# Kernel optimization log

Measured on AMD Instinct MI355X. Metric: run time of the kernel, lower is better.

## Reference

```python
import jax, jax.numpy as jnp
import numpy as np

NUM_EXPERTS = 16
TOP_K = 2
FFT_LEN = 512
SEQ_LEN = 512
PRED_LEN = 720
MOE_TEMP = 1.0


def setup_inputs() -> dict:
    key = jax.random.key(0)
    ks = jax.random.split(key, 5)
    x = jax.random.normal(ks[0], (8192, SEQ_LEN), dtype=jnp.float32)
    # gating network: Linear(fft_len//2 -> num_experts)
    gw = jax.random.normal(ks[1], (NUM_EXPERTS, FFT_LEN // 2), dtype=jnp.float32) * (1.0 / np.sqrt(FFT_LEN // 2))
    gb = jnp.zeros((NUM_EXPERTS,), dtype=jnp.float32)
    # experts: RLinear = instance-norm (RevIN) + Linear(seq->pred), stacked
    ew = jax.random.normal(ks[2], (NUM_EXPERTS, SEQ_LEN, PRED_LEN), dtype=jnp.float32) * (1.0 / np.sqrt(SEQ_LEN))
    eb = jnp.zeros((NUM_EXPERTS, PRED_LEN), dtype=jnp.float32)
    return {"x": x, "gw": gw, "gb": gb, "ew": ew, "eb": eb}


def periodogram(x, n):
    # x: [B, L] -> normalized power spectrum [B, n//2]
    x0 = x - jnp.mean(x, axis=1, keepdims=True)
    dft = jnp.fft.fft(x0, n=n, axis=1) / jnp.sqrt(jnp.asarray(n, x.dtype))
    I = jnp.abs(dft[:, : n // 2]) ** 2
    s = jnp.sum(I, axis=1, keepdims=True)
    s = jnp.where(s == 0, 1.0, s)
    return I / s


def expert_apply(x, ew, eb):
    # RLinear: instance normalize, linear map, de-normalize
    mu = jnp.mean(x, axis=1, keepdims=True)
    sd = jnp.std(x, axis=1, keepdims=True) + 1e-5
    xn = (x - mu) / sd  # [B, L]
    # all experts densely: [B,L] x [E,L,P] -> [E,B,P]
    y = jnp.einsum('bl,elp->ebp', xn, ew) + eb[:, None, :]
    return y * sd[None] + mu[None]  # [E, B, P]


def reference(x, gw, gb, ew, eb):
    I = periodogram(x, FFT_LEN)  # [B, n//2]
    gate = (I @ gw.T + gb) / MOE_TEMP  # eval mode: divide by temp, no noise
    topk_vals, topk_idx = jax.lax.top_k(gate, TOP_K)  # [B, k]
    gates = jax.nn.softmax(topk_vals, axis=1)  # [B, k]
    expert_out = expert_apply(x, ew, eb)  # [E, B, P]
    # gather selected experts: [B, k, P]
    sel = jnp.take_along_axis(
        jnp.transpose(expert_out, (1, 0, 2)), topk_idx[:, :, None], axis=1
    )
    return jnp.sum(gates[:, :, None] * sel, axis=1)  # [B, P]
```

## Files before the change

### kernel.cpp

```cpp
#include <hip/hip_runtime.h>
#include <hip/hip_bf16.h>
#include <math.h>

#define NEXP  16
#define SEQ   512
#define PRED  720
#define NROWS 8192
#define NFREQ 256

typedef __bf16 bf16x8 __attribute__((ext_vector_type(8)));
typedef float  f32x16 __attribute__((ext_vector_type(16)));

__device__ __forceinline__ void gload_lds16(const void* g, void* l) {
    __builtin_amdgcn_global_load_lds(
        (const __attribute__((address_space(1))) unsigned int*)g,
        (__attribute__((address_space(3))) unsigned int*)l, 16, 0, 0);
}

__device__ __forceinline__ int xcd_swizzle(int bid, int nwg) {
    const int q = nwg >> 3, r = nwg & 7;
    const int xcd = bid & 7, off = bid >> 3;
    return (xcd < r ? xcd * (q + 1) : r * (q + 1) + (xcd - r) * q) + off;
}

__global__ __launch_bounds__(256) void k_preproc(const float* __restrict__ ew,
                                                 const float* __restrict__ x,
                                                 __hip_bfloat16* __restrict__ ewt,
                                                 __hip_bfloat16* __restrict__ bthi,
                                                 __hip_bfloat16* __restrict__ btlo,
                                                 __hip_bfloat16* __restrict__ xn,
                                                 __hip_bfloat16* __restrict__ xnlo,
                                                 float* __restrict__ meta,
                                                 int* __restrict__ nredo)
{
    const int bid = blockIdx.x;
    const int t   = threadIdx.x;

    if (bid < 512) {
        if (bid == 0 && t == 0) *nredo = 0;
        const int tid  = bid * 256 + t;
        const int f    = tid >> 9;
        const int lidx = tid & 511;
        const int m    = (f * lidx) & 511;

        constexpr double Cj[9] = {0.9999247018391445033, 0.9996988186962042201,
                                  0.9987954562051723927, 0.9951847266721968862,
                                  0.9807852804032304491, 0.9238795325112867561,
                                  0.7071067811865475244, 0.0, -1.0};
        constexpr double Sj[9] = {0.0122715382857199261, 0.0245412285229122880,
                                  0.0490676743274180143, 0.0980171403295606020,
                                  0.1950903220161282678, 0.3826834323650897717,
                                  0.7071067811865475244, 1.0, 0.0};
        double cr = 1.0, ci = 0.0;
#pragma unroll
        for (int j = 0; j < 9; ++j) {
            const bool on = (m >> j) & 1;
            const double mr = on ? Cj[j] : 1.0;
            const double mi = on ? Sj[j] : 0.0;
            const double nr = cr * mr - ci * mi;
            ci = cr * mi + ci * mr;
            cr = nr;
        }
        const size_t c0 = (size_t)(2 * f) * 512 + lidx;
        const size_t c1 = (size_t)(2 * f + 1) * 512 + lidx;
        {
            __hip_bfloat16 h = __float2bfloat16((float)cr);
            float hif = __bfloat162float(h);
            bthi[c0] = h;
            btlo[c0] = __float2bfloat16((float)(cr - (double)hif));
        }
        {
            __hip_bfloat16 h = __float2bfloat16((float)ci);
            float hif = __bfloat162float(h);
            bthi[c1] = h;
            btlo[c1] = __float2bfloat16((float)(ci - (double)hif));
        }
        return;
    }

    if (bid < 6400) {
        __shared__ float tile[32][33];
        const int rel = bid - 512;
        const int e   = rel / 368;
        const int rem = rel % 368;
        const int p0  = (rem % 23) * 32;
        const int l0  = (rem / 23) * 32;
        const int tx  = t & 31;
        const int ty  = t >> 5;
        const float* src = ew + (size_t)e * SEQ * PRED;
#pragma unroll
        for (int i = 0; i < 4; ++i) {
            int l = l0 + ty + i * 8;
            int p = p0 + tx;
            tile[ty + i * 8][tx] = (p < PRED) ? src[(size_t)l * PRED + p] : 0.f;
        }
        __syncthreads();
        __hip_bfloat16* dst = ewt + (size_t)e * PRED * SEQ;
#pragma unroll
        for (int i = 0; i < 4; ++i) {
            int p = p0 + ty + i * 8;
            int l = l0 + tx;
            if (p < PRED) dst[(size_t)p * SEQ + l] = __float2bfloat16(tile[tx][ty + i * 8]);
        }
        return;
    }

    {
        const int wv = t >> 6, l = t & 63;
        const int b  = (bid - 6400) * 4 + wv;
        const float* xr = x + (size_t)b * SEQ;

        const float4 v0 = *(const float4*)(xr + l * 8);
        const float4 v1 = *(const float4*)(xr + l * 8 + 4);
        const double d0 = v0.x, d1 = v0.y, d2 = v0.z, d3 = v0.w;
        const double d4 = v1.x, d5 = v1.y, d6 = v1.z, d7 = v1.w;

        double s1 = ((d0 + d1) + (d2 + d3)) + ((d4 + d5) + (d6 + d7));
        double s2 = ((d0 * d0 + d1 * d1) + (d2 * d2 + d3 * d3)) +
                    ((d4 * d4 + d5 * d5) + (d6 * d6 + d7 * d7));
#pragma unroll
        for (int off = 1; off < 64; off <<= 1) {
            s1 += __shfl_xor(s1, off);
            s2 += __shfl_xor(s2, off);
        }
        const double mu = s1 * (1.0 / 512.0);
        double var = s2 * (1.0 / 512.0) - mu * mu;
        if (var < 0.0) var = 0.0;
        const double sd = sqrt(var) + 1e-5, inv = 1.0 / sd;

        unsigned int hw[4], lw[4];
#define CONV(j, dj)                                                         \
        {                                                                   \
            double xnd = (dj - mu) * inv;                                   \
            __hip_bfloat16 h = __float2bfloat16((float)xnd);                \
            float hif = __bfloat162float(h);                                \
            __hip_bfloat16 lo = __float2bfloat16((float)(xnd - (double)hif)); \
            unsigned int hb = *(unsigned short*)&h;                         \
            unsigned int lb = *(unsigned short*)&lo;                        \
            if ((j & 1) == 0) { hw[j >> 1] = hb; lw[j >> 1] = lb; }         \
            else { hw[j >> 1] |= hb << 16; lw[j >> 1] |= lb << 16; }        \
        }
        CONV(0, d0) CONV(1, d1) CONV(2, d2) CONV(3, d3)
        CONV(4, d4) CONV(5, d5) CONV(6, d6) CONV(7, d7)
#undef CONV
        *(uint4*)(xn   + (size_t)b * SEQ + l * 8) = uint4{hw[0], hw[1], hw[2], hw[3]};
        *(uint4*)(xnlo + (size_t)b * SEQ + l * 8) = uint4{lw[0], lw[1], lw[2], lw[3]};

        if (l == 0) {
            meta[b * 4 + 0] = (float)mu;
            meta[b * 4 + 3] = (float)sd;
        }
    }
}

__global__ __launch_bounds__(256, 3) void k_dft_gemm(
    const __hip_bfloat16* __restrict__ xn, const __hip_bfloat16* __restrict__ xnlo,
    const __hip_bfloat16* __restrict__ bthi, const __hip_bfloat16* __restrict__ btlo,
    float* __restrict__ Iout)
{
    const int wgid = xcd_swizzle(blockIdx.x, 512);
    const int rt = wgid >> 2;
    const int ct = wgid & 3;

    __shared__ __align__(16) __hip_bfloat16 As[2][64][64];
    __shared__ __align__(16) __hip_bfloat16 Bs[2][128][64];

    const int t  = threadIdx.x;
    const int wv = t >> 6, l = t & 63;

    size_t aoff[2], boff[4];
    int arow[2], achk[2], brow[4], bchk[4];
#pragma unroll
    for (int i = 0; i < 2; ++i) {
        const int idx = i * 256 + t;
        const int row = idx >> 3, chk = idx & 7;
        const int swz = (row & 7) ^ ((row & 8) >> 1);
        arow[i] = row; achk[i] = chk;
        aoff[i] = (size_t)(rt * 64 + row) * SEQ + (size_t)(chk ^ swz) * 8;
    }
#pragma unroll
    for (int i = 0; i < 4; ++i) {
        const int idx = i * 256 + t;
        const int row = idx >> 3, chk = idx & 7;
        const int swz = (row & 7) ^ ((row & 8) >> 1);
        brow[i] = row; bchk[i] = chk;
        boff[i] = (size_t)(ct * 128 + row) * SEQ + (size_t)(chk ^ swz) * 8;
    }

#define DSTAGE(buf, kk) do {                                                   \
    const int pass_ = (kk) >> 3;                                               \
    const int koff_ = ((kk) & 7) * 64;                                         \
    const __hip_bfloat16* ap_ = (pass_ == 1) ? xnlo : xn;                      \
    const __hip_bfloat16* bp_ = (pass_ == 2) ? btlo : bthi;                    \
    _Pragma("unroll")                                                          \
    for (int i_ = 0; i_ < 2; ++i_)                                             \
        gload_lds16(ap_ + aoff[i_] + koff_, &As[buf][arow[i_]][achk[i_] * 8]); \
    _Pragma("unroll")                                                          \
    for (int i_ = 0; i_ < 4; ++i_)                                             \
        gload_lds16(bp_ + boff[i_] + koff_, &Bs[buf][brow[i_]][bchk[i_] * 8]); \
} while (0)

    f32x16 acc[2];
#pragma unroll
    for (int ni = 0; ni < 2; ++ni)
#pragma unroll
        for (int q = 0; q < 16; ++q) acc[ni][q] = 0.f;

    const int wr = wv >> 1, wc = wv & 1;
    const int fl = l & 31, fh = l >> 5;
    const int rswz = (fl & 7) ^ ((fl & 8) >> 1);

    DSTAGE(0, 0);
    asm volatile("s_waitcnt vmcnt(0)" ::: "memory");
    __builtin_amdgcn_s_barrier();
#pragma unroll
    for (int kt = 0; kt < 24; ++kt) {
        const int cur = kt & 1;
        if (kt < 23) DSTAGE(cur ^ 1, kt + 1);
        __builtin_amdgcn_sched_barrier(0);
        __builtin_amdgcn_s_setprio(1);
#pragma unroll
        for (int ks = 0; ks < 4; ++ks) {
            const int cc = ((ks * 2 + fh) ^ rswz) * 8;
            const bf16x8 a  = *(const bf16x8*)&As[cur][wr * 32 + fl][cc];
            const bf16x8 b0 = *(const bf16x8*)&Bs[cur][wc * 64 + fl][cc];
            const bf16x8 b1 = *(const bf16x8*)&Bs[cur][wc * 64 + 32 + fl][cc];
            acc[0] = __builtin_amdgcn_mfma_f32_32x32x16_bf16(a, b0, acc[0], 0, 0, 0);
            acc[1] = __builtin_amdgcn_mfma_f32_32x32x16_bf16(a, b1, acc[1], 0, 0, 0);
        }
        __builtin_amdgcn_s_setprio(0);
        __builtin_amdgcn_sched_barrier(0);
        asm volatile("s_waitcnt vmcnt(0)" ::: "memory");
        __builtin_amdgcn_s_barrier();
    }
#undef DSTAGE

    const int crow_base = 4 * fh;
#pragma unroll
    for (int ni = 0; ni < 2; ++ni) {
        const int col = ct * 128 + wc * 64 + ni * 32 + fl;
#pragma unroll
        for (int q = 0; q < 16; ++q) {
            const float v = acc[ni][q];
            const float w = __shfl_xor(v, 1);
            if ((fl & 1) == 0) {
                const int rl = wr * 32 + (q & 3) + 8 * (q >> 2) + crow_base;
                Iout[(size_t)(rt * 64 + rl) * NFREQ + (col >> 1)] = v * v + w * w;
            }
        }
    }
}

__global__ __launch_bounds__(256) void k_gatefin(const float* __restrict__ Iout,
                                                 const float* __restrict__ gw,
                                                 const float* __restrict__ gb,
                                                 float* __restrict__ meta,
                                                 int* __restrict__ eidx,
                                                 int* __restrict__ redo,
                                                 int* __restrict__ nredo)
{
    __shared__ float gws[NEXP * 257];
    __shared__ float Pw[4][256];
    __shared__ float Gs[4][16];

    const int t  = threadIdx.x;
    const int wv = t >> 6, l = t & 63;
    const int b  = blockIdx.x * 4 + wv;

    for (int i = t; i < NEXP * NFREQ; i += 256)
        gws[(i >> 8) * 257 + (i & 255)] = gw[i];
    __syncthreads();

    const float* Ir = Iout + (size_t)b * NFREQ;
    const float i0 = Ir[l], i1 = Ir[64 + l], i2 = Ir[128 + l], i3 = Ir[192 + l];
    Pw[wv][l] = i0; Pw[wv][64 + l] = i1; Pw[wv][128 + l] = i2; Pw[wv][192 + l] = i3;
    float ps = (i0 + i1) + (i2 + i3);
#pragma unroll
    for (int off = 1; off < 64; off <<= 1) ps += __shfl_xor(ps, off);

    const int e = l >> 2, kb = l & 3;
    float acc = 0.f;
#pragma unroll 8
    for (int j = 0; j < 64; ++j) {
        const int k = kb + 4 * j;
        acc += Pw[wv][k] * gws[e * 257 + k];
    }
    acc += __shfl_xor(acc, 1);
    acc += __shfl_xor(acc, 2);
    if (kb == 0) Gs[wv][e] = acc;

    if (l == 0) {
        const float sdiv  = (ps == 0.f) ? 1.f : ps;
        const float inv_s = 1.f / sdiv;
        float b1 = -1e30f, b2 = -1e30f, b3 = -1e30f;
        int i1b = 0, i2b = 0;
#pragma unroll
        for (int i = 0; i < NEXP; ++i) {
            float v = Gs[wv][i] * inv_s + gb[i];
            if (v > b1)      { b3 = b2; b2 = b1; i2b = i1b; b1 = v; i1b = i; }
            else if (v > b2) { b3 = b2; b2 = v; i2b = i; }
            else if (v > b3) { b3 = v; }
        }
        if (b2 - b3 < 1e-4f * fmaxf(1.f, fabsf(b1))) {
            const int r = atomicAdd(nredo, 1);
            redo[r] = b;
        } else {
            const float sd = meta[b * 4 + 3];
            const float ee = __expf(b2 - b1);
            const float w0 = 1.f / (1.f + ee);
            const float w1 = ee / (1.f + ee);
            meta[b * 4 + 1] = w0 * sd;
            meta[b * 4 + 2] = w1 * sd;
            eidx[b * 2 + 0] = i1b;
            eidx[b * 2 + 1] = i2b;
        }
    }
}

__global__ __launch_bounds__(256, 4) void k_gate64(const float* __restrict__ x,
                                                   const float* __restrict__ gw,
                                                   const float* __restrict__ gb,
                                                   float* __restrict__ meta,
                                                   int* __restrict__ eidx,
                                                   const int* __restrict__ redo,
                                                   const int* __restrict__ nredo)
{
    __shared__ double Pw[4][256];
    __shared__ double Gs[4][16];

    const int t  = threadIdx.x;
    const int wv = t >> 6, l = t & 63;
    const int n  = *nredo;

    for (int it = blockIdx.x * 4 + wv; it < n; it += gridDim.x * 4) {
        const int b = redo[it];
        const float* xr = x + (size_t)b * SEQ;

        double s1 = 0.0, s2 = 0.0;
#define DLOADV(n_) double vr##n_ = (double)xr[64 * n_ + l]; s1 += vr##n_; s2 += vr##n_ * vr##n_;
        DLOADV(0) DLOADV(1) DLOADV(2) DLOADV(3) DLOADV(4) DLOADV(5) DLOADV(6) DLOADV(7)
#undef DLOADV
        double vi0, vi1, vi2, vi3, vi4, vi5, vi6, vi7;

#pragma unroll
        for (int off = 1; off < 64; off <<= 1) {
            s1 += __shfl_xor(s1, off);
            s2 += __shfl_xor(s2, off);
        }
        const double mu = s1 * (1.0 / 512.0);
        double var = s2 * (1.0 / 512.0) - mu * mu;
        if (var < 0.0) var = 0.0;
        const double sd = sqrt(var) + 1e-5;

#define DSUB(n_) vr##n_ -= mu;
        DSUB(0) DSUB(1) DSUB(2) DSUB(3) DSUB(4) DSUB(5) DSUB(6) DSUB(7)
#undef DSUB

        {
            const double C = 0.70710678118654752440084436210485;
            double a0 = vr0 + vr4, a1 = vr1 + vr5, a2 = vr2 + vr6, a3 = vr3 + vr7;
            double d0 = vr0 - vr4, d1 = vr1 - vr5, d2 = vr2 - vr6, d3 = vr3 - vr7;
            double c0 = a0 + a2, c2 = a0 - a2, c1 = a1 + a3;
            double c3i = a3 - a1;
            double e1r = C * (d1 - d3), e1i = -C * (d1 + d3);
            vr0 = c0 + c1;   vi0 = 0.0;
            vr1 = c0 - c1;   vi1 = 0.0;
            vr2 = c2;        vi2 = c3i;
            vr3 = c2;        vi3 = -c3i;
            vr4 = d0 + e1r;  vi4 = -d2 + e1i;
            vr5 = d0 - e1r;  vi5 = -d2 - e1i;
            vr6 = d0 - e1r;  vi6 =  d2 + e1i;
            vr7 = d0 + e1r;  vi7 =  d2 - e1i;
        }

        double w1r = 1.0, w1i = 0.0;
        {
            constexpr double Cr[6] = {0.9999247018391445033, 0.9996988186962042201,
                                      0.9987954562051723927, 0.9951847266721968862,
                                      0.9807852804032304491, 0.9238795325112867561};
            constexpr double Ci[6] = {-0.0122715382857199261, -0.0245412285229122880,
                                      -0.0490676743274180143, -0.0980171403295606020,
                                      -0.1950903220161282678, -0.3826834323650897717};
#pragma unroll
            for (int j = 0; j < 6; ++j) {
                const bool on = (l >> j) & 1;
                const double mr = on ? Cr[j] : 1.0;
                const double mi = on ? Ci[j] : 0.0;
                const double nr = w1r * mr - w1i * mi;
                w1i = w1r * mi + w1i * mr;
                w1r = nr;
            }
        }

        {
            double wkr = w1r, wki = w1i;
#define DTWID(n_) { double tr_ = vr##n_ * wkr - vi##n_ * wki; \
                    vi##n_ = vr##n_ * wki + vi##n_ * wkr; vr##n_ = tr_; }
#define DWSTEP() { double nr_ = wkr * w1r - wki * w1i; \
                   wki = wkr * w1i + wki * w1r; wkr = nr_; }
            DTWID(4) DWSTEP() DTWID(2) DWSTEP() DTWID(6) DWSTEP() DTWID(1)
            DWSTEP() DTWID(5) DWSTEP() DTWID(3) DWSTEP() DTWID(7)
#undef DTWID
#undef DWSTEP
        }

        double twr, twi;
        {
            double w2r = w1r * w1r - w1i * w1i, w2i = 2.0 * w1r * w1i;
            double w4r = w2r * w2r - w2i * w2i, w4i = 2.0 * w2r * w2i;
            twr = w4r * w4r - w4i * w4i; twi = 2.0 * w4r * w4i;
        }
#define DBF(R, I, h, hi, ter, tei) { \
        double br_ = __shfl_xor(R, h); double bi_ = __shfl_xor(I, h); \
        double dr_ = hi ? (R - br_) : (R + br_); \
        double di_ = hi ? (I - bi_) : (I + bi_); \
        R = dr_ * ter - di_ * tei; I = dr_ * tei + di_ * ter; }
#define DSTG(hc) { \
        const bool hi_ = (l & hc) != 0; \
        const double ter_ = hi_ ? twr : 1.0; \
        const double tei_ = hi_ ? twi : 0.0; \
        DBF(vr0, vi0, hc, hi_, ter_, tei_) DBF(vr1, vi1, hc, hi_, ter_, tei_) \
        DBF(vr2, vi2, hc, hi_, ter_, tei_) DBF(vr3, vi3, hc, hi_, ter_, tei_) \
        DBF(vr4, vi4, hc, hi_, ter_, tei_) DBF(vr5, vi5, hc, hi_, ter_, tei_) \
        DBF(vr6, vi6, hc, hi_, ter_, tei_) DBF(vr7, vi7, hc, hi_, ter_, tei_) \
        double ntr_ = twr * twr - twi * twi; twi = 2.0 * twr * twi; twr = ntr_; }
        DSTG(32) DSTG(16) DSTG(8) DSTG(4) DSTG(2) DSTG(1)
#undef DSTG
#undef DBF

        const int k2 = (int)(__brev((unsigned)l) >> 26);
        double ps = 0.0;
        if ((l & 1) == 0) {
            const int kb = 8 * k2;
            double P;
            P = vr0 * vr0 + vi0 * vi0; ps += P; Pw[wv][0 + kb] = P;
            P = vr1 * vr1 + vi1 * vi1; ps += P; Pw[wv][4 + kb] = P;
            P = vr2 * vr2 + vi2 * vi2; ps += P; Pw[wv][2 + kb] = P;
            P = vr3 * vr3 + vi3 * vi3; ps += P; Pw[wv][6 + kb] = P;
            P = vr4 * vr4 + vi4 * vi4; ps += P; Pw[wv][1 + kb] = P;
            P = vr5 * vr5 + vi5 * vi5; ps += P; Pw[wv][5 + kb] = P;
            P = vr6 * vr6 + vi6 * vi6; ps += P; Pw[wv][3 + kb] = P;
            P = vr7 * vr7 + vi7 * vi7; ps += P; Pw[wv][7 + kb] = P;
        }
#pragma unroll
        for (int off = 1; off < 64; off <<= 1) ps += __shfl_xor(ps, off);

        {
            const int e = l >> 2, kb = l & 3;
            double acc = 0.0;
#pragma unroll 8
            for (int j = 0; j < 64; ++j) {
                int k = kb + 4 * j;
                acc += Pw[wv][k] * (double)gw[e * NFREQ + k];
            }
            acc += __shfl_xor(acc, 1);
            acc += __shfl_xor(acc, 2);
            if (kb == 0) Gs[wv][e] = acc;
        }

        if (l == 0) {
            const double sdiv  = (ps == 0.0) ? 1.0 : ps;
            const double inv_s = 1.0 / sdiv;
            double best = -1e300, best2 = -1e300;
            int i0b = 0, i1b = 0;
#pragma unroll
            for (int i = 0; i < NEXP; ++i) {
                double v = Gs[wv][i] * inv_s + (double)gb[i];
                if (v > best)       { best2 = best; i1b = i0b; best = v; i0b = i; }
                else if (v > best2) { best2 = v; i1b = i; }
            }
            const double eexp = (double)__expf((float)(best2 - best));
            const double w0 = 1.0 / (1.0 + eexp);
            const double w1 = eexp / (1.0 + eexp);
            meta[b * 4 + 0] = (float)mu;
            meta[b * 4 + 1] = (float)(w0 * sd);
            meta[b * 4 + 2] = (float)(w1 * sd);
            meta[b * 4 + 3] = (float)sd;
            eidx[b * 2 + 0] = i0b;
            eidx[b * 2 + 1] = i1b;
        }
    }
}

__global__ __launch_bounds__(256) void k_count(const int* __restrict__ eidx,
                                               int* __restrict__ blockHist)
{
    __shared__ int h[32];
    const int t   = threadIdx.x;
    const int blk = blockIdx.x;
    if (t < 32) h[t] = 0;
    __syncthreads();
    const int b  = blk * 256 + t;
    const int e0 = eidx[2 * b];
    const int e1 = eidx[2 * b + 1];
    atomicAdd(&h[e0], 1);
    atomicAdd(&h[16 + e1], 1);
    __syncthreads();
    if (t < 32) blockHist[(t >> 4) * 512 + blk * 16 + (t & 15)] = h[t];
}

__global__ void k_scan(const int* __restrict__ blockHist, int* __restrict__ counts,
                       int* __restrict__ offs, int* __restrict__ tdesc,
                       int* __restrict__ base)
{
    __shared__ int cnt[32];
    __shared__ int off_s[32];
    const int j = threadIdx.x;
    if (j < 32) {
        const int s = j >> 4, e = j & 15;
        int acc = 0;
        for (int blk = 0; blk < 32; ++blk) acc += blockHist[s * 512 + blk * 16 + e];
        cnt[j] = acc;
        counts[j] = acc;
    }
    __syncthreads();
    if (j < 2) {
        int acc = 0, tt = 0;
        for (int i = 0; i < NEXP; ++i) {
            const int c = cnt[j * 16 + i];
            off_s[j * 16 + i] = acc;
            offs[j * 16 + i]  = acc;
            acc += c;
            const int nt = (c + 63) >> 6;
            for (int k = 0; k < nt; ++k) tdesc[j * 160 + tt++] = (i << 16) | k;
        }
        for (; tt < 160; ++tt) tdesc[j * 160 + tt] = -1;
    }
    __syncthreads();
    if (j < 32) {
        const int s = j >> 4, e = j & 15;
        int run = off_s[j];
        for (int blk = 0; blk < 32; ++blk) {
            base[s * 512 + blk * 16 + e] = run;
            run += blockHist[s * 512 + blk * 16 + e];
        }
    }
}

__global__ __launch_bounds__(256) void k_scatter(const int* __restrict__ eidx,
                                                 const int* __restrict__ base,
                                                 int* __restrict__ lists)
{
    __shared__ int whist[2][4][16];
    const int t   = threadIdx.x;
    const int wv  = t >> 6, l = t & 63;
    const int blk = blockIdx.x;
    const int b   = blk * 256 + t;
    const int e0  = eidx[2 * b];
    const int e1  = eidx[2 * b + 1];
    const unsigned long long before = (1ULL << l) - 1ULL;

    unsigned long long m0 = 0, m1 = 0;
#pragma unroll
    for (int bb = 0; bb < 16; ++bb) {
        unsigned long long m = __ballot(e0 == bb);
        if (e0 == bb) m0 = m;
        if (l == 0) whist[0][wv][bb] = __popcll(m);
    }
#pragma unroll
    for (int bb = 0; bb < 16; ++bb) {
        unsigned long long m = __ballot(e1 == bb);
        if (e1 == bb) m1 = m;
        if (l == 0) whist[1][wv][bb] = __popcll(m);
    }
    __syncthreads();

    int p0 = __popcll(m0 & before);
    int p1 = __popcll(m1 & before);
    for (int w = 0; w < 4; ++w) {
        if (w < wv) {
            p0 += whist[0][w][e0];
            p1 += whist[1][w][e1];
        }
    }
    lists[base[blk * 16 + e0] + p0]                 = b;
    lists[NROWS + base[512 + blk * 16 + e1] + p1]   = b;
}

__global__ __launch_bounds__(256, 3) void k_expert_gemm(
    const __hip_bfloat16* __restrict__ xn, const __hip_bfloat16* __restrict__ ewt,
    const float* __restrict__ eb, const float* __restrict__ meta,
    const int* __restrict__ lists, const int* __restrict__ offs,
    const int* __restrict__ counts, const int* __restrict__ tdesc,
    float* __restrict__ out, float* __restrict__ out2)
{
    const int wgid = xcd_swizzle(blockIdx.x, 1920);
    const int slot = wgid / 960;
    const int rem  = wgid - slot * 960;
    const int tid  = rem / 6;
    const int ct   = rem % 6;
    const int d    = tdesc[slot * 160 + tid];
    if (d < 0) return;
    const int e  = d >> 16;
    const int rt = d & 0xffff;
    const int n_e = counts[slot * NEXP + e];

    __shared__ __align__(16) __hip_bfloat16 As[2][64][64];
    __shared__ __align__(16) __hip_bfloat16 Bs[2][128][64];
    __shared__ int   rowB[64];
    __shared__ float rowMu[64];
    __shared__ float rowC[64];

    const int t  = threadIdx.x;
    const int wv = t >> 6, l = t & 63;
    const int* list = lists + slot * NROWS + offs[slot * NEXP + e];
    if (t < 64) {
        int r  = rt * 64 + t;
        int bb = (r < n_e) ? list[r] : -1;
        rowB[t]  = bb;
        rowMu[t] = (bb >= 0) ? meta[bb * 4] : 0.f;
        rowC[t]  = (bb >= 0) ? meta[bb * 4 + 1 + slot] : 0.f;
    }
    __syncthreads();

    const __hip_bfloat16* asrc[2];
    const __hip_bfloat16* bsrc[4];
    int arow[2], achk[2], brow[4], bchk[4];
#pragma unroll
    for (int i = 0; i < 2; ++i) {
        const int idx = i * 256 + t;
        const int row = idx >> 3, chk = idx & 7;
        const int swz = (row & 7) ^ ((row & 8) >> 1);
        arow[i] = row; achk[i] = chk;
        const int ab = rowB[row];
        asrc[i] = xn + ((ab >= 0) ? (size_t)ab * SEQ : 0) + (size_t)(chk ^ swz) * 8;
    }
#pragma unroll
    for (int i = 0; i < 4; ++i) {
        const int idx = i * 256 + t;
        const int row = idx >> 3, chk = idx & 7;
        const int swz = (row & 7) ^ ((row & 8) >> 1);
        brow[i] = row; bchk[i] = chk;
        const int gc  = ct * 128 + row;
        const int gcc = (gc < PRED) ? gc : (PRED - 1);
        bsrc[i] = ewt + ((size_t)e * PRED + gcc) * SEQ + (size_t)(chk ^ swz) * 8;
    }

#define STAGE(buf, koff) do {                                                  \
    _Pragma("unroll")                                                          \
    for (int i_ = 0; i_ < 2; ++i_)                                             \
        gload_lds16(asrc[i_] + (koff), &As[buf][arow[i_]][achk[i_] * 8]);      \
    _Pragma("unroll")                                                          \
    for (int i_ = 0; i_ < 4; ++i_)                                             \
        gload_lds16(bsrc[i_] + (koff), &Bs[buf][brow[i_]][bchk[i_] * 8]);      \
} while (0)

    f32x16 acc[2];
#pragma unroll
    for (int ni = 0; ni < 2; ++ni)
#pragma unroll
        for (int q = 0; q < 16; ++q) acc[ni][q] = 0.f;

    const int wr = wv >> 1, wc = wv & 1;
    const int fl = l & 31, fh = l >> 5;
    const int rswz = (fl & 7) ^ ((fl & 8) >> 1);

    STAGE(0, 0);
    asm volatile("s_waitcnt vmcnt(0)" ::: "memory");
    __builtin_amdgcn_s_barrier();
#pragma unroll
    for (int kt = 0; kt < 8; ++kt) {
        const int cur = kt & 1;
        if (kt < 7) STAGE(cur ^ 1, (kt + 1) * 64);
        __builtin_amdgcn_sched_barrier(0);
        __builtin_amdgcn_s_setprio(1);
#pragma unroll
        for (int ks = 0; ks < 4; ++ks) {
            const int cc = ((ks * 2 + fh) ^ rswz) * 8;
            const bf16x8 a  = *(const bf16x8*)&As[cur][wr * 32 + fl][cc];
            const bf16x8 b0 = *(const bf16x8*)&Bs[cur][wc * 64 + fl][cc];
            const bf16x8 b1 = *(const bf16x8*)&Bs[cur][wc * 64 + 32 + fl][cc];
            acc[0] = __builtin_amdgcn_mfma_f32_32x32x16_bf16(a, b0, acc[0], 0, 0, 0);
            acc[1] = __builtin_amdgcn_mfma_f32_32x32x16_bf16(a, b1, acc[1], 0, 0, 0);
        }
        __builtin_amdgcn_s_setprio(0);
        __builtin_amdgcn_sched_barrier(0);
        asm volatile("s_waitcnt vmcnt(0)" ::: "memory");
        __builtin_amdgcn_s_barrier();
    }
#undef STAGE

    const int crow_base = 4 * fh;
#pragma unroll
    for (int ni = 0; ni < 2; ++ni) {
        const int col = ct * 128 + wc * 64 + ni * 32 + fl;
        const bool cok = (col < PRED);
        const float ebv = cok ? eb[e * PRED + col] : 0.f;
#pragma unroll
        for (int q = 0; q < 16; ++q) {
            const int rl = wr * 32 + (q & 3) + 8 * (q >> 2) + crow_base;
            const int bb = rowB[rl];
            if (!cok || bb < 0) continue;
            const float v = acc[ni][q] + ebv;
            if (slot == 0) out [(size_t)bb * PRED + col] = rowMu[rl] + rowC[rl] * v;
            else           out2[(size_t)bb * PRED + col] = rowC[rl] * v;
        }
    }
}

__global__ __launch_bounds__(256) void k_merge(float* __restrict__ out,
                                               const float* __restrict__ out2)
{
    const int i = blockIdx.x * 256 + threadIdx.x;
    float4 a = ((float4*)out)[i];
    const float4 b = ((const float4*)out2)[i];
    a.x += b.x; a.y += b.y; a.z += b.z; a.w += b.w;
    ((float4*)out)[i] = a;
}

extern "C" void kernel_launch(void* const* d_in, const int* in_sizes, int n_in,
                              void* d_out, int out_size, void* d_ws, size_t ws_size,
                              hipStream_t stream)
{
    const float* x  = (const float*)d_in[0];
    const float* gw = (const float*)d_in[1];
    const float* gb = (const float*)d_in[2];
    const float* ew = (const float*)d_in[3];
    const float* eb = (const float*)d_in[4];
    float* out = (float*)d_out;
    char*  ws  = (char*)d_ws;

    constexpr size_t XN_OFF   = 0;
    constexpr size_t XN_SZ    = (size_t)NROWS * SEQ * 2;
    constexpr size_t XNLO_OFF = XN_OFF + XN_SZ;
    constexpr size_t EWT_OFF  = XNLO_OFF + XN_SZ;
    constexpr size_t EWT_SZ   = (size_t)NEXP * PRED * SEQ * 2;
    constexpr size_t BTHI_OFF = EWT_OFF + EWT_SZ;
    constexpr size_t BT_SZ    = (size_t)512 * 512 * 2;
    constexpr size_t BTLO_OFF = BTHI_OFF + BT_SZ;
    constexpr size_t IOUT_OFF = BTLO_OFF + BT_SZ;
    constexpr size_t IOUT_SZ  = (size_t)NROWS * NFREQ * 4;
    constexpr size_t META_OFF = IOUT_OFF + IOUT_SZ;
    constexpr size_t META_SZ  = (size_t)NROWS * 4 * 4;
    constexpr size_t EIDX_OFF = META_OFF + META_SZ;
    constexpr size_t EIDX_SZ  = (size_t)NROWS * 2 * 4;
    constexpr size_t LIST_OFF = EIDX_OFF + EIDX_SZ;
    constexpr size_t LIST_SZ  = (size_t)2 * NROWS * 4;
    constexpr size_t CNT_OFF  = LIST_OFF + LIST_SZ;
    constexpr size_t OFFS_OFF = CNT_OFF + 144;
    constexpr size_t TDSC_OFF = OFFS_OFF + 128;
    constexpr size_t BH_OFF   = TDSC_OFF + 1280;
    constexpr size_t BASE_OFF = BH_OFF + 4096;
    constexpr size_t REDO_OFF = BASE_OFF + 4096;
    constexpr size_t OUT2_OFF = REDO_OFF + (size_t)NROWS * 4;

    __hip_bfloat16* xn   = (__hip_bfloat16*)(ws + XN_OFF);
    __hip_bfloat16* xnlo = (__hip_bfloat16*)(ws + XNLO_OFF);
    __hip_bfloat16* ewt  = (__hip_bfloat16*)(ws + EWT_OFF);
    __hip_bfloat16* bthi = (__hip_bfloat16*)(ws + BTHI_OFF);
    __hip_bfloat16* btlo = (__hip_bfloat16*)(ws + BTLO_OFF);
    float* Iout  = (float*)(ws + IOUT_OFF);
    float* meta  = (float*)(ws + META_OFF);
    int* eidx    = (int*)(ws + EIDX_OFF);
    int* lists   = (int*)(ws + LIST_OFF);
    int* counts  = (int*)(ws + CNT_OFF);
    int* nredo   = (int*)(ws + CNT_OFF + 128);
    int* offs    = (int*)(ws + OFFS_OFF);
    int* tdesc   = (int*)(ws + TDSC_OFF);
    int* bhist   = (int*)(ws + BH_OFF);
    int* base    = (int*)(ws + BASE_OFF);
    int* redo    = (int*)(ws + REDO_OFF);
    float* out2  = (float*)(ws + OUT2_OFF);

    k_preproc<<<dim3(8448), dim3(256), 0, stream>>>(ew, x, ewt, bthi, btlo,
                                                    xn, xnlo, meta, nredo);
    k_dft_gemm<<<dim3(512), dim3(256), 0, stream>>>(xn, xnlo, bthi, btlo, Iout);
    k_gatefin<<<dim3(NROWS / 4), dim3(256), 0, stream>>>(Iout, gw, gb, meta, eidx,
                                                         redo, nredo);
    k_gate64<<<dim3(64), dim3(256), 0, stream>>>(x, gw, gb, meta, eidx, redo, nredo);
    k_count<<<dim3(32), dim3(256), 0, stream>>>(eidx, bhist);
    k_scan<<<dim3(1), dim3(64), 0, stream>>>(bhist, counts, offs, tdesc, base);
    k_scatter<<<dim3(32), dim3(256), 0, stream>>>(eidx, base, lists);
    k_expert_gemm<<<dim3(1920), dim3(256), 0, stream>>>(
        xn, ewt, eb, meta, lists, offs, counts, tdesc, out, out2);
    k_merge<<<dim3(NROWS * PRED / 1024), dim3(256), 0, stream>>>(out, out2);
}
```

Measured before the change: 141.4 us.

## Drop LDS staging in GEMMs, merge expert outputs via atomics, batch gate rows

Both MFMA GEMMs stop staging tiles through LDS with double-buffered direct-to-LDS loads and instead load bf16x8 fragments straight from global memory into registers. The separate out2 buffer and merge kernel are replaced by zeroing the output in the preprocessing kernel and accumulating both expert slots with float atomicAdd. The gating kernel now handles four rows per wave with a quarter of the blocks, so the gate-weight LDS fill is amortised over more rows. The launch-bound occupancy hints are relaxed. The changes remove a kernel launch and LDS/barrier overhead, but give up operand reuse across waves and add atomic traffic.

```diff
diff --git a/kernel.cpp b/kernel.cpp
--- a/kernel.cpp
+++ b/kernel.cpp
@@ -10,12 +10,6 @@
 
 typedef __bf16 bf16x8 __attribute__((ext_vector_type(8)));
 typedef float  f32x16 __attribute__((ext_vector_type(16)));
-
-__device__ __forceinline__ void gload_lds16(const void* g, void* l) {
-    __builtin_amdgcn_global_load_lds(
-        (const __attribute__((address_space(1))) unsigned int*)g,
-        (__attribute__((address_space(3))) unsigned int*)l, 16, 0, 0);
-}
 
 __device__ __forceinline__ int xcd_swizzle(int bid, int nwg) {
     const int q = nwg >> 3, r = nwg & 7;
@@ -31,7 +25,8 @@
                                                  __hip_bfloat16* __restrict__ xn,
                                                  __hip_bfloat16* __restrict__ xnlo,
                                                  float* __restrict__ meta,
-                                                 int* __restrict__ nredo)
+                                                 int* __restrict__ nredo,
+                                                 float* __restrict__ out)
 {
     const int bid = blockIdx.x;
     const int t   = threadIdx.x;
@@ -105,7 +100,7 @@
         return;
     }
 
-    {
+    if (bid < 8448) {
         const int wv = t >> 6, l = t & 63;
         const int b  = (bid - 6400) * 4 + wv;
         const float* xr = x + (size_t)b * SEQ;
@@ -150,10 +145,19 @@
             meta[b * 4 + 0] = (float)mu;
             meta[b * 4 + 3] = (float)sd;
         }
-    }
-}
-
-__global__ __launch_bounds__(256, 3) void k_dft_gemm(
+        return;
+    }
+
+    {
+        const size_t base = ((size_t)(bid - 8448) * 256 + t) * 16;
+        float4 z = {0.f, 0.f, 0.f, 0.f};
+#pragma unroll
+        for (int i = 0; i < 4; ++i)
+            *(float4*)(out + base + i * 4) = z;
+    }
+}
+
+__global__ __launch_bounds__(256) void k_dft_gemm(
     const __hip_bfloat16* __restrict__ xn, const __hip_bfloat16* __restrict__ xnlo,
     const __hip_bfloat16* __restrict__ bthi, const __hip_bfloat16* __restrict__ btlo,
     float* __restrict__ Iout)
@@ -162,78 +166,44 @@
     const int rt = wgid >> 2;
     const int ct = wgid & 3;
 
-    __shared__ __align__(16) __hip_bfloat16 As[2][64][64];
-    __shared__ __align__(16) __hip_bfloat16 Bs[2][128][64];
-
     const int t  = threadIdx.x;
     const int wv = t >> 6, l = t & 63;
-
-    size_t aoff[2], boff[4];
-    int arow[2], achk[2], brow[4], bchk[4];
-#pragma unroll
-    for (int i = 0; i < 2; ++i) {
-        const int idx = i * 256 + t;
-        const int row = idx >> 3, chk = idx & 7;
-        const int swz = (row & 7) ^ ((row & 8) >> 1);
-        arow[i] = row; achk[i] = chk;
-        aoff[i] = (size_t)(rt * 64 + row) * SEQ + (size_t)(chk ^ swz) * 8;
-    }
-#pragma unroll
-    for (int i = 0; i < 4; ++i) {
-        const int idx = i * 256 + t;
-        const int row = idx >> 3, chk = idx & 7;
-        const int swz = (row & 7) ^ ((row & 8) >> 1);
-        brow[i] = row; bchk[i] = chk;
-        boff[i] = (size_t)(ct * 128 + row) * SEQ + (size_t)(chk ^ swz) * 8;
-    }
-
-#define DSTAGE(buf, kk) do {                                                   \
-    const int pass_ = (kk) >> 3;                                               \
-    const int koff_ = ((kk) & 7) * 64;                                         \
-    const __hip_bfloat16* ap_ = (pass_ == 1) ? xnlo : xn;                      \
-    const __hip_bfloat16* bp_ = (pass_ == 2) ? btlo : bthi;                    \
-    _Pragma("unroll")                                                          \
-    for (int i_ = 0; i_ < 2; ++i_)                                             \
-        gload_lds16(ap_ + aoff[i_] + koff_, &As[buf][arow[i_]][achk[i_] * 8]); \
-    _Pragma("unroll")                                                          \
-    for (int i_ = 0; i_ < 4; ++i_)                                             \
-        gload_lds16(bp_ + boff[i_] + koff_, &Bs[buf][brow[i_]][bchk[i_] * 8]); \
-} while (0)
-
-    f32x16 acc[2];
-#pragma unroll
-    for (int ni = 0; ni < 2; ++ni)
-#pragma unroll
-        for (int q = 0; q < 16; ++q) acc[ni][q] = 0.f;
-
     const int wr = wv >> 1, wc = wv & 1;
     const int fl = l & 31, fh = l >> 5;
-    const int rswz = (fl & 7) ^ ((fl & 8) >> 1);
-
-    DSTAGE(0, 0);
-    asm volatile("s_waitcnt vmcnt(0)" ::: "memory");
-    __builtin_amdgcn_s_barrier();
-#pragma unroll
-    for (int kt = 0; kt < 24; ++kt) {
-        const int cur = kt & 1;
-        if (kt < 23) DSTAGE(cur ^ 1, kt + 1);
-        __builtin_amdgcn_sched_barrier(0);
-        __builtin_amdgcn_s_setprio(1);
-#pragma unroll
-        for (int ks = 0; ks < 4; ++ks) {
-            const int cc = ((ks * 2 + fh) ^ rswz) * 8;
-            const bf16x8 a  = *(const bf16x8*)&As[cur][wr * 32 + fl][cc];
-            const bf16x8 b0 = *(const bf16x8*)&Bs[cur][wc * 64 + fl][cc];
-            const bf16x8 b1 = *(const bf16x8*)&Bs[cur][wc * 64 + 32 + fl][cc];
-            acc[0] = __builtin_amdgcn_mfma_f32_32x32x16_bf16(a, b0, acc[0], 0, 0, 0);
-            acc[1] = __builtin_amdgcn_mfma_f32_32x32x16_bf16(a, b1, acc[1], 0, 0, 0);
-        }
-        __builtin_amdgcn_s_setprio(0);
-        __builtin_amdgcn_sched_barrier(0);
-        asm volatile("s_waitcnt vmcnt(0)" ::: "memory");
-        __builtin_amdgcn_s_barrier();
-    }
-#undef DSTAGE
+
+    const int arow = rt * 64 + wr * 32 + fl;
+    const size_t arow_off = (size_t)arow * SEQ + fh * 8;
+    const int col0 = ct * 128 + wc * 64 + fl;
+    const int col1 = col0 + 32;
+    const size_t b0_off = (size_t)col0 * SEQ + fh * 8;
+    const size_t b1_off = (size_t)col1 * SEQ + fh * 8;
+
+    f32x16 acc[2];
+#pragma unroll
+    for (int ni = 0; ni < 2; ++ni)
+#pragma unroll
+        for (int q = 0; q < 16; ++q) acc[ni][q] = 0.f;
+
+#pragma unroll
+    for (int pass = 0; pass < 3; ++pass) {
+        const __hip_bfloat16* ap = (pass == 1) ? xnlo : xn;
+        const __hip_bfloat16* bp = (pass == 2) ? btlo : bthi;
+        const __hip_bfloat16* apr = ap + arow_off;
+        const __hip_bfloat16* bp0 = bp + b0_off;
+        const __hip_bfloat16* bp1 = bp + b1_off;
+#pragma unroll 2
+        for (int kk = 0; kk < 8; ++kk) {
+#pragma unroll
+            for (int ks = 0; ks < 4; ++ks) {
+                const int koff = kk * 64 + ks * 16;
+                const bf16x8 a  = *(const bf16x8*)(apr + koff);
+                const bf16x8 b0 = *(const bf16x8*)(bp0 + koff);
+                const bf16x8 b1 = *(const bf16x8*)(bp1 + koff);
+                acc[0] = __builtin_amdgcn_mfma_f32_32x32x16_bf16(a, b0, acc[0], 0, 0, 0);
+                acc[1] = __builtin_amdgcn_mfma_f32_32x32x16_bf16(a, b1, acc[1], 0, 0, 0);
+            }
+        }
+    }
 
     const int crow_base = 4 * fh;
 #pragma unroll
@@ -265,54 +235,56 @@
 
     const int t  = threadIdx.x;
     const int wv = t >> 6, l = t & 63;
-    const int b  = blockIdx.x * 4 + wv;
 
     for (int i = t; i < NEXP * NFREQ; i += 256)
         gws[(i >> 8) * 257 + (i & 255)] = gw[i];
     __syncthreads();
 
-    const float* Ir = Iout + (size_t)b * NFREQ;
-    const float i0 = Ir[l], i1 = Ir[64 + l], i2 = Ir[128 + l], i3 = Ir[192 + l];
-    Pw[wv][l] = i0; Pw[wv][64 + l] = i1; Pw[wv][128 + l] = i2; Pw[wv][192 + l] = i3;
-    float ps = (i0 + i1) + (i2 + i3);
-#pragma unroll
-    for (int off = 1; off < 64; off <<= 1) ps += __shfl_xor(ps, off);
-
-    const int e = l >> 2, kb = l & 3;
-    float acc = 0.f;
+    for (int r = 0; r < 4; ++r) {
+        const int b = blockIdx.x * 16 + wv * 4 + r;
+        const float* Ir = Iout + (size_t)b * NFREQ;
+        const float i0 = Ir[l], i1 = Ir[64 + l], i2 = Ir[128 + l], i3 = Ir[192 + l];
+        Pw[wv][l] = i0; Pw[wv][64 + l] = i1; Pw[wv][128 + l] = i2; Pw[wv][192 + l] = i3;
+        float ps = (i0 + i1) + (i2 + i3);
+#pragma unroll
+        for (int off = 1; off < 64; off <<= 1) ps += __shfl_xor(ps, off);
+
+        const int e = l >> 2, kb = l & 3;
+        float acc = 0.f;
 #pragma unroll 8
-    for (int j = 0; j < 64; ++j) {
-        const int k = kb + 4 * j;
-        acc += Pw[wv][k] * gws[e * 257 + k];
-    }
-    acc += __shfl_xor(acc, 1);
-    acc += __shfl_xor(acc, 2);
-    if (kb == 0) Gs[wv][e] = acc;
-
-    if (l == 0) {
-        const float sdiv  = (ps == 0.f) ? 1.f : ps;
-        const float inv_s = 1.f / sdiv;
-        float b1 = -1e30f, b2 = -1e30f, b3 = -1e30f;
-        int i1b = 0, i2b = 0;
-#pragma unroll
-        for (int i = 0; i < NEXP; ++i) {
-            float v = Gs[wv][i] * inv_s + gb[i];
-            if (v > b1)      { b3 = b2; b2 = b1; i2b = i1b; b1 = v; i1b = i; }
-            else if (v > b2) { b3 = b2; b2 = v; i2b = i; }
-            else if (v > b3) { b3 = v; }
-        }
-        if (b2 - b3 < 1e-4f * fmaxf(1.f, fabsf(b1))) {
-            const int r = atomicAdd(nredo, 1);
-            redo[r] = b;
-        } else {
-            const float sd = meta[b * 4 + 3];
-            const float ee = __expf(b2 - b1);
-            const float w0 = 1.f / (1.f + ee);
-            const float w1 = ee / (1.f + ee);
-            meta[b * 4 + 1] = w0 * sd;
-            meta[b * 4 + 2] = w1 * sd;
-            eidx[b * 2 + 0] = i1b;
-            eidx[b * 2 + 1] = i2b;
+        for (int j = 0; j < 64; ++j) {
+            const int k = kb + 4 * j;
+            acc += Pw[wv][k] * gws[e * 257 + k];
+        }
+        acc += __shfl_xor(acc, 1);
+        acc += __shfl_xor(acc, 2);
+        if (kb == 0) Gs[wv][e] = acc;
+
+        if (l == 0) {
+            const float sdiv  = (ps == 0.f) ? 1.f : ps;
+            const float inv_s = 1.f / sdiv;
+            float b1 = -1e30f, b2 = -1e30f, b3 = -1e30f;
+            int i1b = 0, i2b = 0;
+#pragma unroll
+            for (int i = 0; i < NEXP; ++i) {
+                float v = Gs[wv][i] * inv_s + gb[i];
+                if (v > b1)      { b3 = b2; b2 = b1; i2b = i1b; b1 = v; i1b = i; }
+                else if (v > b2) { b3 = b2; b2 = v; i2b = i; }
+                else if (v > b3) { b3 = v; }
+            }
+            if (b2 - b3 < 1e-4f * fmaxf(1.f, fabsf(b1))) {
+                const int rr = atomicAdd(nredo, 1);
+                redo[rr] = b;
+            } else {
+                const float sd = meta[b * 4 + 3];
+                const float ee = __expf(b2 - b1);
+                const float w0 = 1.f / (1.f + ee);
+                const float w1 = ee / (1.f + ee);
+                meta[b * 4 + 1] = w0 * sd;
+                meta[b * 4 + 2] = w1 * sd;
+                eidx[b * 2 + 0] = i1b;
+                eidx[b * 2 + 1] = i2b;
+            }
         }
     }
 }
@@ -577,12 +549,12 @@
     lists[NROWS + base[512 + blk * 16 + e1] + p1]   = b;
 }
 
-__global__ __launch_bounds__(256, 3) void k_expert_gemm(
+__global__ __launch_bounds__(256) void k_expert_gemm(
     const __hip_bfloat16* __restrict__ xn, const __hip_bfloat16* __restrict__ ewt,
     const float* __restrict__ eb, const float* __restrict__ meta,
     const int* __restrict__ lists, const int* __restrict__ offs,
     const int* __restrict__ counts, const int* __restrict__ tdesc,
-    float* __restrict__ out, float* __restrict__ out2)
+    float* __restrict__ out)
 {
     const int wgid = xcd_swizzle(blockIdx.x, 1920);
     const int slot = wgid / 960;
@@ -595,8 +567,6 @@
     const int rt = d & 0xffff;
     const int n_e = counts[slot * NEXP + e];
 
-    __shared__ __align__(16) __hip_bfloat16 As[2][64][64];
-    __shared__ __align__(16) __hip_bfloat16 Bs[2][128][64];
     __shared__ int   rowB[64];
     __shared__ float rowMu[64];
     __shared__ float rowC[64];
@@ -613,72 +583,37 @@
     }
     __syncthreads();
 
-    const __hip_bfloat16* asrc[2];
-    const __hip_bfloat16* bsrc[4];
-    int arow[2], achk[2], brow[4], bchk[4];
-#pragma unroll
-    for (int i = 0; i < 2; ++i) {
-        const int idx = i * 256 + t;
-        const int row = idx >> 3, chk = idx & 7;
-        const int swz = (row & 7) ^ ((row & 8) >> 1);
-        arow[i] = row; achk[i] = chk;
-        const int ab = rowB[row];
-        asrc[i] = xn + ((ab >= 0) ? (size_t)ab * SEQ : 0) + (size_t)(chk ^ swz) * 8;
-    }
-#pragma unroll
-    for (int i = 0; i < 4; ++i) {
-        const int idx = i * 256 + t;
-        const int row = idx >> 3, chk = idx & 7;
-        const int swz = (row & 7) ^ ((row & 8) >> 1);
-        brow[i] = row; bchk[i] = chk;
-        const int gc  = ct * 128 + row;
-        const int gcc = (gc < PRED) ? gc : (PRED - 1);
-        bsrc[i] = ewt + ((size_t)e * PRED + gcc) * SEQ + (size_t)(chk ^ swz) * 8;
-    }
-
-#define STAGE(buf, koff) do {                                                  \
-    _Pragma("unroll")                                                          \
-    for (int i_ = 0; i_ < 2; ++i_)                                             \
-        gload_lds16(asrc[i_] + (koff), &As[buf][arow[i_]][achk[i_] * 8]);      \
-    _Pragma("unroll")                                                          \
-    for (int i_ = 0; i_ < 4; ++i_)                                             \
-        gload_lds16(bsrc[i_] + (koff), &Bs[buf][brow[i_]][bchk[i_] * 8]);      \
-} while (0)
-
-    f32x16 acc[2];
-#pragma unroll
-    for (int ni = 0; ni < 2; ++ni)
-#pragma unroll
-        for (int q = 0; q < 16; ++q) acc[ni][q] = 0.f;
-
     const int wr = wv >> 1, wc = wv & 1;
     const int fl = l & 31, fh = l >> 5;
-    const int rswz = (fl & 7) ^ ((fl & 8) >> 1);
-
-    STAGE(0, 0);
-    asm volatile("s_waitcnt vmcnt(0)" ::: "memory");
-    __builtin_amdgcn_s_barrier();
-#pragma unroll
-    for (int kt = 0; kt < 8; ++kt) {
-        const int cur = kt & 1;
-        if (kt < 7) STAGE(cur ^ 1, (kt + 1) * 64);
-        __builtin_amdgcn_sched_barrier(0);
-        __builtin_amdgcn_s_setprio(1);
+
+    const int myrow = rowB[wr * 32 + fl];
+    const __hip_bfloat16* apr =
+        xn + ((myrow >= 0) ? (size_t)myrow * SEQ : 0) + fh * 8;
+    const int col0 = ct * 128 + wc * 64 + fl;
+    const int col1 = col0 + 32;
+    const __hip_bfloat16* bp0 =
+        ewt + ((size_t)e * PRED + ((col0 < PRED) ? col0 : (PRED - 1))) * SEQ + fh * 8;
+    const __hip_bfloat16* bp1 =
+        ewt + ((size_t)e * PRED + ((col1 < PRED) ? col1 : (PRED - 1))) * SEQ + fh * 8;
+
+    f32x16 acc[2];
+#pragma unroll
+    for (int ni = 0; ni < 2; ++ni)
+#pragma unroll
+        for (int q = 0; q < 16; ++q) acc[ni][q] = 0.f;
+
+#pragma unroll 2
+    for (int kk = 0; kk < 8; ++kk) {
 #pragma unroll
         for (int ks = 0; ks < 4; ++ks) {
-            const int cc = ((ks * 2 + fh) ^ rswz) * 8;
-            const bf16x8 a  = *(const bf16x8*)&As[cur][wr * 32 + fl][cc];
-            const bf16x8 b0 = *(const bf16x8*)&Bs[cur][wc * 64 + fl][cc];
-            const bf16x8 b1 = *(const bf16x8*)&Bs[cur][wc * 64 + 32 + fl][cc];
+            const int koff = kk * 64 + ks * 16;
+            const bf16x8 a  = *(const bf16x8*)(apr + koff);
+            const bf16x8 b0 = *(const bf16x8*)(bp0 + koff);
+            const bf16x8 b1 = *(const bf16x8*)(bp1 + koff);
             acc[0] = __builtin_amdgcn_mfma_f32_32x32x16_bf16(a, b0, acc[0], 0, 0, 0);
             acc[1] = __builtin_amdgcn_mfma_f32_32x32x16_bf16(a, b1, acc[1], 0, 0, 0);
         }
-        __builtin_amdgcn_s_setprio(0);
-        __builtin_amdgcn_sched_barrier(0);
-        asm volatile("s_waitcnt vmcnt(0)" ::: "memory");
-        __builtin_amdgcn_s_barrier();
-    }
-#undef STAGE
+    }
 
     const int crow_base = 4 * fh;
 #pragma unroll
@@ -692,20 +627,11 @@
             const int bb = rowB[rl];
             if (!cok || bb < 0) continue;
             const float v = acc[ni][q] + ebv;
-            if (slot == 0) out [(size_t)bb * PRED + col] = rowMu[rl] + rowC[rl] * v;
-            else           out2[(size_t)bb * PRED + col] = rowC[rl] * v;
-        }
-    }
-}
-
-__global__ __launch_bounds__(256) void k_merge(float* __restrict__ out,
-                                               const float* __restrict__ out2)
-{
-    const int i = blockIdx.x * 256 + threadIdx.x;
-    float4 a = ((float4*)out)[i];
-    const float4 b = ((const float4*)out2)[i];
-    a.x += b.x; a.y += b.y; a.z += b.z; a.w += b.w;
-    ((float4*)out)[i] = a;
+            const float contrib = (slot == 0) ? (rowMu[rl] + rowC[rl] * v)
+                                              : (rowC[rl] * v);
+            atomicAdd(out + (size_t)bb * PRED + col, contrib);
+        }
+    }
 }
 
 extern "C" void kernel_launch(void* const* d_in, const int* in_sizes, int n_in,
@@ -742,7 +668,6 @@
     constexpr size_t BH_OFF   = TDSC_OFF + 1280;
     constexpr size_t BASE_OFF = BH_OFF + 4096;
     constexpr size_t REDO_OFF = BASE_OFF + 4096;
-    constexpr size_t OUT2_OFF = REDO_OFF + (size_t)NROWS * 4;
 
     __hip_bfloat16* xn   = (__hip_bfloat16*)(ws + XN_OFF);
     __hip_bfloat16* xnlo = (__hip_bfloat16*)(ws + XNLO_OFF);
@@ -760,18 +685,16 @@
     int* bhist   = (int*)(ws + BH_OFF);
     int* base    = (int*)(ws + BASE_OFF);
     int* redo    = (int*)(ws + REDO_OFF);
-    float* out2  = (float*)(ws + OUT2_OFF);
-
-    k_preproc<<<dim3(8448), dim3(256), 0, stream>>>(ew, x, ewt, bthi, btlo,
-                                                    xn, xnlo, meta, nredo);
+
+    k_preproc<<<dim3(9888), dim3(256), 0, stream>>>(ew, x, ewt, bthi, btlo,
+                                                    xn, xnlo, meta, nredo, out);
     k_dft_gemm<<<dim3(512), dim3(256), 0, stream>>>(xn, xnlo, bthi, btlo, Iout);
-    k_gatefin<<<dim3(NROWS / 4), dim3(256), 0, stream>>>(Iout, gw, gb, meta, eidx,
-                                                         redo, nredo);
+    k_gatefin<<<dim3(NROWS / 16), dim3(256), 0, stream>>>(Iout, gw, gb, meta, eidx,
+                                                          redo, nredo);
     k_gate64<<<dim3(64), dim3(256), 0, stream>>>(x, gw, gb, meta, eidx, redo, nredo);
     k_count<<<dim3(32), dim3(256), 0, stream>>>(eidx, bhist);
     k_scan<<<dim3(1), dim3(64), 0, stream>>>(bhist, counts, offs, tdesc, base);
     k_scatter<<<dim3(32), dim3(256), 0, stream>>>(eidx, base, lists);
     k_expert_gemm<<<dim3(1920), dim3(256), 0, stream>>>(
-        xn, ewt, eb, meta, lists, offs, counts, tdesc, out, out2);
-    k_merge<<<dim3(NROWS * PRED / 1024), dim3(256), 0, stream>>>(out, out2);
-}
+        xn, ewt, eb, meta, lists, offs, counts, tdesc, out);
+}
```

Result: slower. 257.6 us (+82.2%).
